# Performance work log

Hardware: AMD Instinct MI355X
Metric: run time of the kernel (lower is better)

## Reference

```python
import jax, jax.numpy as jnp
import numpy as np
import math

HID = 768
HEADS = 12
HEAD_DIM = HID // HEADS
B, L = 64, 1024


def _xavier(key, shape):
    fan_in, fan_out = shape[0], shape[1]
    lim = math.sqrt(6.0 / (fan_in + fan_out))
    return jax.random.uniform(key, shape, jnp.float32, -lim, lim)


def setup_inputs() -> dict:
    key = jax.random.key(0)
    ks = jax.random.split(key, 12)
    inp = {
        "x_img": jax.random.normal(ks[0], (B, L, HID), jnp.float32),
        "cond": jax.random.normal(ks[1], (B, HID), jnp.float32),
        # attention projections
        "wq": _xavier(ks[2], (HID, HID)), "bq": jnp.zeros((HID,), jnp.float32),
        "wk": _xavier(ks[3], (HID, HID)), "bk": jnp.zeros((HID,), jnp.float32),
        "wv": _xavier(ks[4], (HID, HID)), "bv": jnp.zeros((HID,), jnp.float32),
        "wo": _xavier(ks[5], (HID, HID)), "bo": jnp.zeros((HID,), jnp.float32),
        # adaLN: zero-initialized in the original (keep small random so grads are non-trivial? No — stay faithful: zero init is the module's init, but zero would kill modulation. Use small random for a meaningful test.)
        "w_ada": jax.random.normal(ks[6], (HID, 6 * HID), jnp.float32) * 0.02,
        "b_ada": jnp.zeros((6 * HID,), jnp.float32),
        # MLP
        "w1": _xavier(ks[7], (HID, HID)), "b1": jnp.zeros((HID,), jnp.float32),
        "w2": _xavier(ks[8], (HID, HID)), "b2": jnp.zeros((HID,), jnp.float32),
        # LayerNorm params (norm_1: default scale=1, bias init const 1; norm_2: scale init const 1, bias default 0)
        "ln1_scale": jnp.ones((HID,), jnp.float32), "ln1_bias": jnp.ones((HID,), jnp.float32),
        "ln2_scale": jnp.ones((HID,), jnp.float32), "ln2_bias": jnp.zeros((HID,), jnp.float32),
    }
    return inp


def _layernorm(x, scale, bias, eps=1e-6):
    mu = jnp.mean(x, axis=-1, keepdims=True)
    var = jnp.var(x, axis=-1, keepdims=True)
    return (x - mu) * jax.lax.rsqrt(var + eps) * scale + bias


def _modulate(x, shift, scale):
    # shift/scale: [B, H] -> broadcast over seq axis
    return x * (1.0 + scale[:, None, :]) + shift[:, None, :]


def _attention(x, wq, bq, wk, bk, wv, bv, wo, bo):
    q = x @ wq + bq
    k = x @ wk + bk
    v = x @ wv + bv
    def split(t):
        b, l, _ = t.shape
        return t.reshape(b, l, HEADS, HEAD_DIM).transpose(0, 2, 1, 3)  # b h l d
    q, k, v = split(q), split(k), split(v)
    logits = jnp.einsum("bhqd,bhkd->bhqk", q, k) / math.sqrt(HEAD_DIM)
    attn = jax.nn.softmax(logits, axis=-1)
    out = jnp.einsum("bhqk,bhkd->bhqd", attn, v)
    out = out.transpose(0, 2, 1, 3).reshape(x.shape)  # b l (h d)
    return out @ wo + bo


def reference(x_img, cond, wq, bq, wk, bk, wv, bv, wo, bo, w_ada, b_ada,
              w1, b1, w2, b2, ln1_scale, ln1_bias, ln2_scale, ln2_bias):
    c = jax.nn.silu(cond) @ w_ada + b_ada  # [B, 6H]
    shift_msa, scale_msa, gate_msa, shift_mlp, scale_mlp, gate_mlp = jnp.split(c, 6, axis=1)

    h = _modulate(_layernorm(x_img, ln1_scale, ln1_bias), shift_msa, scale_msa)
    attn_out = _attention(h, wq, bq, wk, bk, wv, bv, wo, bo)
    x = x_img + gate_msa[:, None, :] * attn_out

    h2 = _modulate(_layernorm(x, ln2_scale, ln2_bias), shift_mlp, scale_mlp)
    mlp_out = jax.nn.silu(h2 @ w1 + b1) @ w2 + b2
    x = x + gate_mlp[:, None, :] * mlp_out
    return x
```

## Files before the change

### kernel.cpp

```cpp
#include <hip/hip_runtime.h>
#include <hip/hip_bf16.h>

typedef __bf16 bf16x8 __attribute__((ext_vector_type(8)));
typedef __bf16 bf16x4 __attribute__((ext_vector_type(4)));
typedef float  f32x4  __attribute__((ext_vector_type(4)));

#define MFMA_BF16(A_, B_, C_) __builtin_amdgcn_mfma_f32_16x16x32_bf16(A_, B_, C_, 0, 0, 0)

static constexpr int    HIDC  = 768;
static constexpr int    BB    = 64;
static constexpr int    LL    = 1024;
static constexpr int    MROWS = BB * LL;
static constexpr int    NHEAD = 12;
static constexpr int    HD    = 64;
static constexpr size_t QKV1  = (size_t)BB * NHEAD * LL * HD;

static constexpr size_t OFF_WQKVT = 0;
static constexpr size_t OFF_WOT   = OFF_WQKVT + (size_t)2304 * 768 * 2;
static constexpr size_t OFF_W1T   = OFF_WOT   + (size_t)768 * 768 * 2;
static constexpr size_t OFF_W2T   = OFF_W1T   + (size_t)768 * 768 * 2;
static constexpr size_t OFF_BQKV  = OFF_W2T   + (size_t)768 * 768 * 2;
static constexpr size_t OFF_C     = OFF_BQKV  + (size_t)2304 * 4;
static constexpr size_t OFF_H     = OFF_C     + (size_t)64 * 4608 * 4;
static constexpr size_t OFF_AO    = OFF_H     + (size_t)MROWS * HIDC * 2;
static constexpr size_t OFF_QKV   = OFF_AO    + (size_t)MROWS * HIDC * 2;

__device__ __forceinline__ void async16(const __bf16* g, __bf16* l) {
    __builtin_amdgcn_global_load_lds((const __attribute__((address_space(1))) void*)g,
                                     (__attribute__((address_space(3))) void*)l, 16, 0, 0);
}

#define PH_BARRIER() do { __builtin_amdgcn_sched_barrier(0); asm volatile("" ::: "memory"); \
    __builtin_amdgcn_s_barrier(); asm volatile("" ::: "memory"); __builtin_amdgcn_sched_barrier(0); } while (0)

__global__ __launch_bounds__(256) void tcvt_k(const float* __restrict__ src, __bf16* __restrict__ dst) {
    int i = blockIdx.x * 256 + threadIdx.x;
    int kk = i / 768, n = i - kk * 768;
    dst[(size_t)n * 768 + kk] = (__bf16)src[i];
}

__global__ __launch_bounds__(256) void bcat_k(const float* __restrict__ bq, const float* __restrict__ bk,
                                              const float* __restrict__ bv, float* __restrict__ bqkv) {
    int i = blockIdx.x * 256 + threadIdx.x;
    if (i < 2304) {
        int w = i / 768, r = i - w * 768;
        const float* p = (w == 0) ? bq : (w == 1) ? bk : bv;
        bqkv[i] = p[r];
    }
}

__global__ __launch_bounds__(256) void ada_k(const float* __restrict__ cond, const float* __restrict__ w_ada,
                                             const float* __restrict__ b_ada, float* __restrict__ c) {
    __shared__ float s[8][768];
    const int tid = threadIdx.x;
    const int bt = blockIdx.x / 18;
    const int nt = blockIdx.x % 18;
    #pragma unroll
    for (int i = 0; i < 24; ++i) {
        int idx = i * 256 + tid;
        int bb = idx / 768, kk = idx - bb * 768;
        float v = cond[(size_t)(bt * 8 + bb) * 768 + kk];
        s[bb][kk] = v / (1.f + __expf(-v));
    }
    __syncthreads();
    const int n = nt * 256 + tid;
    float acc[8];
    #pragma unroll
    for (int j = 0; j < 8; ++j) acc[j] = 0.f;
    for (int k = 0; k < 768; ++k) {
        float w = w_ada[(size_t)k * 4608 + n];
        #pragma unroll
        for (int j = 0; j < 8; ++j) acc[j] += s[j][k] * w;
    }
    float bias = b_ada[n];
    #pragma unroll
    for (int j = 0; j < 8; ++j) c[(size_t)(bt * 8 + j) * 4608 + n] = acc[j] + bias;
}

__global__ __launch_bounds__(256) void ln_mod_k(const float* __restrict__ x,
                                                const float* __restrict__ lns, const float* __restrict__ lnb,
                                                const float* __restrict__ c, int shift_off, int scale_off,
                                                __bf16* __restrict__ out) {
    const int row = blockIdx.x, tid = threadIdx.x;
    const size_t base = (size_t)row * HIDC;
    const int b = row >> 10;
    float v0 = x[base + tid], v1 = x[base + 256 + tid], v2 = x[base + 512 + tid];
    float s = v0 + v1 + v2;
    float ss = v0 * v0 + v1 * v1 + v2 * v2;
    #pragma unroll
    for (int off = 1; off < 64; off <<= 1) { s += __shfl_xor(s, off); ss += __shfl_xor(ss, off); }
    __shared__ float red[8];
    const int wave = tid >> 6, lane = tid & 63;
    if (lane == 0) { red[wave] = s; red[4 + wave] = ss; }
    __syncthreads();
    s  = red[0] + red[1] + red[2] + red[3];
    ss = red[4] + red[5] + red[6] + red[7];
    const float mu   = s * (1.f / 768.f);
    const float var  = ss * (1.f / 768.f) - mu * mu;
    const float rstd = rsqrtf(var + 1e-6f);
    const float* cb = c + (size_t)b * 4608;
    #pragma unroll
    for (int i = 0; i < 3; ++i) {
        int col = i * 256 + tid;
        float v = (i == 0) ? v0 : (i == 1) ? v1 : v2;
        float val = (v - mu) * rstd * lns[col] + lnb[col];
        val = val * (1.f + cb[scale_off + col]) + cb[shift_off + col];
        out[base + col] = (__bf16)val;
    }
}

__global__ __launch_bounds__(256) void vtr_k(const __bf16* __restrict__ v, __bf16* __restrict__ vt) {
    __shared__ __attribute__((aligned(16))) __bf16 t[64][72];
    const int bid = blockIdx.x;
    const int bh = bid >> 4, lt = bid & 15;
    const int l0 = lt * 64;
    const size_t src = (size_t)bh * LL * HD + (size_t)l0 * HD;
    const size_t dst = (size_t)bh * HD * LL + l0;
    const int tid = threadIdx.x;
    const int rA = tid >> 3, cA = (tid & 7) * 8;
    bf16x8 a0 = *(const bf16x8*)(v + src + (size_t)rA * HD + cA);
    bf16x8 a1 = *(const bf16x8*)(v + src + (size_t)(rA + 32) * HD + cA);
    *(bf16x8*)&t[rA][cA] = a0;
    *(bf16x8*)&t[rA + 32][cA] = a1;
    __syncthreads();
    const int r2 = tid & 31, dg = tid >> 5;
    bf16x8 b0 = *(const bf16x8*)&t[2 * r2][dg * 8];
    bf16x8 b1 = *(const bf16x8*)&t[2 * r2 + 1][dg * 8];
    #pragma unroll
    for (int j = 0; j < 8; ++j) {
        union { __bf16 h[2]; unsigned u; } pk;
        pk.h[0] = b0[j]; pk.h[1] = b1[j];
        *reinterpret_cast<unsigned*>(vt + dst + (size_t)(dg * 8 + j) * LL + 2 * r2) = pk.u;
    }
}

template<int EPI>
__global__ __launch_bounds__(512, 2) void gemm256_k(const __bf16* __restrict__ A, const __bf16* __restrict__ BT,
                                                    const float* __restrict__ bias, int NBLK,
                                                    const float* __restrict__ e_res, const float* __restrict__ e_gate,
                                                    void* __restrict__ out0) {
    constexpr int K = 768;
    constexpr int NKT = K / 64;
    __shared__ __attribute__((aligned(16))) unsigned char LDSB[131072];
    const int tid = threadIdx.x;
    const int nwg = gridDim.x;
    const int cpx = nwg >> 3;
    const int bid = blockIdx.x;
    const int swz = (bid & 7) * cpx + (bid >> 3);
    const int mb = swz / NBLK, nb = swz - mb * NBLK;
    const size_t m0 = (size_t)mb * 256;
    const int n0 = nb * 256;
    const int wave = tid >> 6, lane = tid & 63;
    const int wm = wave >> 2, wn = wave & 3;
    const int lr = lane & 15, lg = lane >> 4;

    int prow[2], pcol[2], pphys[2];
    #pragma unroll
    for (int i = 0; i < 2; ++i) {
        int p = (i * 512 + tid) * 16;
        int Lb = p ^ (((p >> 9) & 1) << 5);
        prow[i] = Lb >> 7;
        pcol[i] = (Lb & 127) >> 1;
        pphys[i] = p;
    }
    auto STAGE = [&](const __bf16* gbase, size_t rowstart, int kt, int regoff) {
        #pragma unroll
        for (int i = 0; i < 2; ++i) {
            const __bf16* g = gbase + (rowstart + (size_t)prow[i]) * K + kt * 64 + pcol[i];
            async16(g, (__bf16*)(LDSB + regoff + pphys[i]));
        }
    };
    auto AFRAG = [&](int db, int mf, int ks) -> bf16x8 {
        int Lb = (mf * 16 + lr) * 128 + ks * 64 + lg * 16;
        int ph = Lb ^ (((Lb >> 9) & 1) << 5);
        return *(const bf16x8*)(LDSB + db * 65536 + wm * 16384 + ph);
    };
    auto BFRAG = [&](int db, int nf, int ks) -> bf16x8 {
        int Lb = ((wn & 1) * 64 + nf * 16 + lr) * 128 + ks * 64 + lg * 16;
        int ph = Lb ^ (((Lb >> 9) & 1) << 5);
        return *(const bf16x8*)(LDSB + db * 65536 + 32768 + (wn >> 1) * 16384 + ph);
    };

    f32x4 acc[8][4];
    #pragma unroll
    for (int i = 0; i < 8; ++i)
        #pragma unroll
        for (int j = 0; j < 4; ++j) acc[i][j] = (f32x4){0.f, 0.f, 0.f, 0.f};
    bf16x8 Af[4][2], Bf[4][2];

    STAGE(BT, (size_t)n0,       0, 32768);
    STAGE(BT, (size_t)n0 + 128, 0, 49152);
    STAGE(A,  m0,               0, 0);
    STAGE(A,  m0 + 128,         0, 16384);
    STAGE(BT, (size_t)n0,       1, 65536 + 32768);
    STAGE(BT, (size_t)n0 + 128, 1, 65536 + 49152);
    asm volatile("s_waitcnt vmcnt(4)" ::: "memory");
    PH_BARRIER();

    #pragma unroll 2
    for (int g = 0; g < NKT; ++g) {
        const int db = g & 1, dbn = db ^ 1;
        if (g + 1 < NKT) STAGE(A, m0, g + 1, dbn * 65536);
        #pragma unroll
        for (int mf = 0; mf < 4; ++mf) { Af[mf][0] = AFRAG(db, mf, 0); Af[mf][1] = AFRAG(db, mf, 1); }
        #pragma unroll
        for (int nf = 0; nf < 2; ++nf) { Bf[nf][0] = BFRAG(db, nf, 0); Bf[nf][1] = BFRAG(db, nf, 1); }
        __builtin_amdgcn_s_setprio(1);
        #pragma unroll
        for (int ks = 0; ks < 2; ++ks)
            #pragma unroll
            for (int mf = 0; mf < 4; ++mf)
                #pragma unroll
                for (int nf = 0; nf < 2; ++nf)
                    acc[mf][nf] = MFMA_BF16(Af[mf][ks], Bf[nf][ks], acc[mf][nf]);
        __builtin_amdgcn_s_setprio(0);
        PH_BARRIER();
        if (g + 1 < NKT) STAGE(A, m0 + 128, g + 1, dbn * 65536 + 16384);
        #pragma unroll
        for (int nf = 2; nf < 4; ++nf) { Bf[nf][0] = BFRAG(db, nf, 0); Bf[nf][1] = BFRAG(db, nf, 1); }
        __builtin_amdgcn_s_setprio(1);
        #pragma unroll
        for (int ks = 0; ks < 2; ++ks)
            #pragma unroll
            for (int mf = 0; mf < 4; ++mf)
                #pragma unroll
                for (int nf = 2; nf < 4; ++nf)
                    acc[mf][nf] = MFMA_BF16(Af[mf][ks], Bf[nf][ks], acc[mf][nf]);
        __builtin_amdgcn_s_setprio(0);
        PH_BARRIER();
        if (g + 2 < NKT) STAGE(BT, (size_t)n0, g + 2, db * 65536 + 32768);
        #pragma unroll
        for (int mf = 0; mf < 4; ++mf) { Af[mf][0] = AFRAG(db, mf + 4, 0); Af[mf][1] = AFRAG(db, mf + 4, 1); }
        __builtin_amdgcn_s_setprio(1);
        #pragma unroll
        for (int ks = 0; ks < 2; ++ks)
            #pragma unroll
            for (int mf = 0; mf < 4; ++mf)
                #pragma unroll
                for (int nf = 0; nf < 2; ++nf)
                    acc[mf + 4][nf] = MFMA_BF16(Af[mf][ks], Bf[nf][ks], acc[mf + 4][nf]);
        __builtin_amdgcn_s_setprio(0);
        PH_BARRIER();
        if (g + 2 < NKT) STAGE(BT, (size_t)n0 + 128, g + 2, db * 65536 + 49152);
        __builtin_amdgcn_s_setprio(1);
        #pragma unroll
        for (int ks = 0; ks < 2; ++ks)
            #pragma unroll
            for (int mf = 0; mf < 4; ++mf)
                #pragma unroll
                for (int nf = 2; nf < 4; ++nf)
                    acc[mf + 4][nf] = MFMA_BF16(Af[mf][ks], Bf[nf][ks], acc[mf + 4][nf]);
        __builtin_amdgcn_s_setprio(0);
        if (g < NKT - 2)       asm volatile("s_waitcnt vmcnt(4)" ::: "memory");
        else if (g == NKT - 2) asm volatile("s_waitcnt vmcnt(0)" ::: "memory");
        if (g + 1 < NKT) PH_BARRIER();
    }

    #pragma unroll
    for (int mf = 0; mf < 8; ++mf) {
        #pragma unroll
        for (int nf = 0; nf < 4; ++nf) {
            #pragma unroll
            for (int r = 0; r < 4; ++r) {
                const int row = wm * 128 + mf * 16 + lg * 4 + r;
                const int col = wn * 64 + nf * 16 + lr;
                const size_t m = m0 + row;
                const int n = n0 + col;
                float val = acc[mf][nf][r] + bias[n];
                if constexpr (EPI == 0) {
                    int which = n / 768, rem = n - which * 768;
                    int hh = rem >> 6, dd = rem & 63;
                    size_t bI = m >> 10, lI = m & 1023;
                    ((__bf16*)out0)[((((size_t)which * BB + bI) * NHEAD + hh) * LL + lI) * HD + dd] = (__bf16)val;
                } else if constexpr (EPI == 1) {
                    size_t bI = m >> 10;
                    float gg = e_gate[bI * 4608 + n];
                    ((float*)out0)[m * HIDC + n] = e_res[m * HIDC + n] + gg * val;
                } else {
                    float sv = val / (1.f + __expf(-val));
                    ((__bf16*)out0)[m * HIDC + n] = (__bf16)sv;
                }
            }
        }
    }
}

__global__ __launch_bounds__(256) void attn_k(const __bf16* __restrict__ qb, const __bf16* __restrict__ kb,
                                              const __bf16* __restrict__ vtg, __bf16* __restrict__ out) {
    __shared__ __attribute__((aligned(16))) __bf16 Kls[64][72];
    __shared__ __attribute__((aligned(16))) __bf16 Vls[64][72];
    const int nwg = gridDim.x;
    const int cpx = nwg >> 3;
    const int bid = blockIdx.x;
    const int swz = (bid & 7) * cpx + (bid >> 3);
    const int bh = swz >> 3;
    const int qt = swz & 7;
    const int b = bh / NHEAD, h = bh - b * NHEAD;
    const int tid = threadIdx.x;
    const int wave = tid >> 6, lane = tid & 63;
    const int lr = lane & 15, lg = lane >> 4;
    const size_t base  = (size_t)bh * LL * HD;
    const size_t baseT = (size_t)bh * HD * LL;

    const int q0 = qt * 128 + wave * 32;
    bf16x8 qf[2][2];
    #pragma unroll
    for (int qi = 0; qi < 2; ++qi) {
        const __bf16* qrow = qb + base + (size_t)(q0 + qi * 16 + lr) * HD;
        qf[qi][0] = *(const bf16x8*)(qrow + lg * 8);
        qf[qi][1] = *(const bf16x8*)(qrow + 32 + lg * 8);
    }

    f32x4 acc[2][4];
    #pragma unroll
    for (int qi = 0; qi < 2; ++qi)
        #pragma unroll
        for (int i = 0; i < 4; ++i) acc[qi][i] = (f32x4){0.f, 0.f, 0.f, 0.f};
    float m_run[2] = {-1e30f, -1e30f}, l_run[2] = {0.f, 0.f};

    const int rA = tid >> 3, cA = (tid & 7) * 8;

    for (int it = 0; it < LL / 64; ++it) {
        const int kv0 = it * 64;
        bf16x8 rk0 = *(const bf16x8*)(kb + base + (size_t)(kv0 + rA) * HD + cA);
        bf16x8 rk1 = *(const bf16x8*)(kb + base + (size_t)(kv0 + rA + 32) * HD + cA);
        bf16x8 rv0 = *(const bf16x8*)(vtg + baseT + (size_t)rA * LL + kv0 + cA);
        bf16x8 rv1 = *(const bf16x8*)(vtg + baseT + (size_t)(rA + 32) * LL + kv0 + cA);
        __syncthreads();
        *(bf16x8*)&Kls[rA][cA] = rk0;
        *(bf16x8*)&Kls[rA + 32][cA] = rk1;
        *(bf16x8*)&Vls[rA][cA] = rv0;
        *(bf16x8*)&Vls[rA + 32][cA] = rv1;
        __syncthreads();

        f32x4 s[2][4];
        #pragma unroll
        for (int sf = 0; sf < 4; ++sf) {
            const bf16x8 kf0 = *(const bf16x8*)&Kls[sf * 16 + lr][lg * 8];
            const bf16x8 kf1 = *(const bf16x8*)&Kls[sf * 16 + lr][32 + lg * 8];
            #pragma unroll
            for (int qi = 0; qi < 2; ++qi) {
                f32x4 t = (f32x4){0.f, 0.f, 0.f, 0.f};
                t = MFMA_BF16(kf0, qf[qi][0], t);
                t = MFMA_BF16(kf1, qf[qi][1], t);
                s[qi][sf] = t;
            }
        }
        float corr[2];
        #pragma unroll
        for (int qi = 0; qi < 2; ++qi) {
            float tm = -1e30f;
            #pragma unroll
            for (int sf = 0; sf < 4; ++sf)
                #pragma unroll
                for (int r = 0; r < 4; ++r) { float v = s[qi][sf][r] * 0.125f; s[qi][sf][r] = v; tm = fmaxf(tm, v); }
            tm = fmaxf(tm, __shfl_xor(tm, 16));
            tm = fmaxf(tm, __shfl_xor(tm, 32));
            const float mnew = fmaxf(m_run[qi], tm);
            corr[qi] = __expf(m_run[qi] - mnew);
            float rs = 0.f;
            #pragma unroll
            for (int sf = 0; sf < 4; ++sf)
                #pragma unroll
                for (int r = 0; r < 4; ++r) { float e = __expf(s[qi][sf][r] - mnew); s[qi][sf][r] = e; rs += e; }
            rs += __shfl_xor(rs, 16);
            rs += __shfl_xor(rs, 32);
            l_run[qi] = l_run[qi] * corr[qi] + rs;
            m_run[qi] = mnew;
            #pragma unroll
            for (int of = 0; of < 4; ++of)
                #pragma unroll
                for (int r = 0; r < 4; ++r) acc[qi][of][r] *= corr[qi];
        }
        #pragma unroll
        for (int ks = 0; ks < 2; ++ks) {
            bf16x8 pb[2];
            #pragma unroll
            for (int qi = 0; qi < 2; ++qi)
                #pragma unroll
                for (int j = 0; j < 4; ++j) {
                    pb[qi][j]     = (__bf16)s[qi][2 * ks][j];
                    pb[qi][4 + j] = (__bf16)s[qi][2 * ks + 1][j];
                }
            #pragma unroll
            for (int of = 0; of < 4; ++of) {
                const bf16x4 v0 = *(const bf16x4*)&Vls[of * 16 + lr][ks * 32 + lg * 4];
                const bf16x4 v1 = *(const bf16x4*)&Vls[of * 16 + lr][ks * 32 + 16 + lg * 4];
                bf16x8 vf;
                #pragma unroll
                for (int j = 0; j < 4; ++j) { vf[j] = v0[j]; vf[4 + j] = v1[j]; }
                #pragma unroll
                for (int qi = 0; qi < 2; ++qi)
                    acc[qi][of] = MFMA_BF16(vf, pb[qi], acc[qi][of]);
            }
        }
    }
    #pragma unroll
    for (int qi = 0; qi < 2; ++qi) {
        const float inv = 1.f / l_run[qi];
        const int qq = q0 + qi * 16 + lr;
        #pragma unroll
        for (int of = 0; of < 4; ++of)
            #pragma unroll
            for (int r = 0; r < 4; ++r) {
                const int d = of * 16 + lg * 4 + r;
                out[((size_t)b * LL + qq) * HIDC + h * HD + d] = (__bf16)(acc[qi][of][r] * inv);
            }
    }
}

extern "C" void kernel_launch(void* const* d_in, const int* in_sizes, int n_in,
                              void* d_out, int out_size, void* d_ws, size_t ws_size,
                              hipStream_t stream) {
    const float* x_img = (const float*)d_in[0];
    const float* cond  = (const float*)d_in[1];
    const float* wq    = (const float*)d_in[2];
    const float* bq    = (const float*)d_in[3];
    const float* wk    = (const float*)d_in[4];
    const float* bk    = (const float*)d_in[5];
    const float* wv    = (const float*)d_in[6];
    const float* bv    = (const float*)d_in[7];
    const float* wo    = (const float*)d_in[8];
    const float* bo    = (const float*)d_in[9];
    const float* w_ada = (const float*)d_in[10];
    const float* b_ada = (const float*)d_in[11];
    const float* w1    = (const float*)d_in[12];
    const float* b1    = (const float*)d_in[13];
    const float* w2    = (const float*)d_in[14];
    const float* b2    = (const float*)d_in[15];
    const float* ln1s  = (const float*)d_in[16];
    const float* ln1b  = (const float*)d_in[17];
    const float* ln2s  = (const float*)d_in[18];
    const float* ln2b  = (const float*)d_in[19];

    char* ws = (char*)d_ws;
    __bf16* wqkvT = (__bf16*)(ws + OFF_WQKVT);
    __bf16* woT   = (__bf16*)(ws + OFF_WOT);
    __bf16* w1T   = (__bf16*)(ws + OFF_W1T);
    __bf16* w2T   = (__bf16*)(ws + OFF_W2T);
    float*  bqkv  = (float*)(ws + OFF_BQKV);
    float*  cbuf  = (float*)(ws + OFF_C);
    __bf16* hbuf  = (__bf16*)(ws + OFF_H);
    __bf16* vtb   = (__bf16*)(ws + OFF_H);
    __bf16* aobuf = (__bf16*)(ws + OFF_AO);
    __bf16* qkv   = (__bf16*)(ws + OFF_QKV);
    float*  xbuf  = (float*)(ws + OFF_QKV);

    dim3 blk(256);
    dim3 blk512(512);

    tcvt_k<<<2304, blk, 0, stream>>>(wq, wqkvT);
    tcvt_k<<<2304, blk, 0, stream>>>(wk, wqkvT + (size_t)768 * 768);
    tcvt_k<<<2304, blk, 0, stream>>>(wv, wqkvT + (size_t)2 * 768 * 768);
    tcvt_k<<<2304, blk, 0, stream>>>(wo, woT);
    tcvt_k<<<2304, blk, 0, stream>>>(w1, w1T);
    tcvt_k<<<2304, blk, 0, stream>>>(w2, w2T);
    bcat_k<<<9, blk, 0, stream>>>(bq, bk, bv, bqkv);
    ada_k<<<144, blk, 0, stream>>>(cond, w_ada, b_ada, cbuf);

    ln_mod_k<<<MROWS, blk, 0, stream>>>(x_img, ln1s, ln1b, cbuf, 0, 768, hbuf);

    gemm256_k<0><<<2304, blk512, 0, stream>>>(hbuf, wqkvT, bqkv, 9, nullptr, nullptr, (void*)qkv);

    vtr_k<<<768 * 16, blk, 0, stream>>>(qkv + 2 * QKV1, vtb);

    attn_k<<<BB * NHEAD * 8, blk, 0, stream>>>(qkv, qkv + QKV1, vtb, aobuf);

    gemm256_k<1><<<768, blk512, 0, stream>>>(aobuf, woT, bo, 3, x_img, cbuf + 2 * 768, (void*)xbuf);

    ln_mod_k<<<MROWS, blk, 0, stream>>>(xbuf, ln2s, ln2b, cbuf, 3 * 768, 4 * 768, hbuf);

    gemm256_k<2><<<768, blk512, 0, stream>>>(hbuf, w1T, b1, 3, nullptr, nullptr, (void*)aobuf);

    gemm256_k<1><<<768, blk512, 0, stream>>>(aobuf, w2T, b2, 3, xbuf, cbuf + 5 * 768, d_out);

    (void)in_sizes; (void)n_in; (void)out_size; (void)ws_size;
}
```

Baseline: 1.349 ms.

## Pipeline attention K/V loads asynchronously, fuse V layout into QKV epilogue, lazy rescale

The QKV GEMM epilogue now pre-scales Q by log2(e)/sqrt(d), so the softmax can use exp2 directly. It also writes V in an MFMA-fragment-friendly tiled layout, which removes the separate V transpose kernel. The attention kernel stages K and V tiles into a 4-deep LDS ring with async global-to-LDS loads, two tiles ahead, and uses an XOR swizzle on K. It skips the running-max rescale when the new max does not exceed the old one by more than a threshold. The six weight-conversion launches are merged into one. The lazy rescale relies on the threshold keeping exp2 values bounded in fp32.

```diff
diff --git a/kernel.cpp b/kernel.cpp
--- a/kernel.cpp
+++ b/kernel.cpp
@@ -2,7 +2,6 @@
 #include <hip/hip_bf16.h>
 
 typedef __bf16 bf16x8 __attribute__((ext_vector_type(8)));
-typedef __bf16 bf16x4 __attribute__((ext_vector_type(4)));
 typedef float  f32x4  __attribute__((ext_vector_type(4)));
 
 #define MFMA_BF16(A_, B_, C_) __builtin_amdgcn_mfma_f32_16x16x32_bf16(A_, B_, C_, 0, 0, 0)
@@ -14,6 +13,8 @@
 static constexpr int    NHEAD = 12;
 static constexpr int    HD    = 64;
 static constexpr size_t QKV1  = (size_t)BB * NHEAD * LL * HD;
+static constexpr float  QSCALE = 0.1803368801111204f;
+static constexpr float  THR2   = 11.5416f;
 
 static constexpr size_t OFF_WQKVT = 0;
 static constexpr size_t OFF_WOT   = OFF_WQKVT + (size_t)2304 * 768 * 2;
@@ -33,10 +34,16 @@
 #define PH_BARRIER() do { __builtin_amdgcn_sched_barrier(0); asm volatile("" ::: "memory"); \
     __builtin_amdgcn_s_barrier(); asm volatile("" ::: "memory"); __builtin_amdgcn_sched_barrier(0); } while (0)
 
-__global__ __launch_bounds__(256) void tcvt_k(const float* __restrict__ src, __bf16* __restrict__ dst) {
-    int i = blockIdx.x * 256 + threadIdx.x;
+__global__ __launch_bounds__(256) void tcvt6_k(const float* __restrict__ s0, const float* __restrict__ s1,
+                                               const float* __restrict__ s2, const float* __restrict__ s3,
+                                               const float* __restrict__ s4, const float* __restrict__ s5,
+                                               __bf16* __restrict__ dbase) {
+    const int widx = blockIdx.x / 2304;
+    const int i = (blockIdx.x % 2304) * 256 + threadIdx.x;
+    const float* src = (widx == 0) ? s0 : (widx == 1) ? s1 : (widx == 2) ? s2
+                     : (widx == 3) ? s3 : (widx == 4) ? s4 : s5;
     int kk = i / 768, n = i - kk * 768;
-    dst[(size_t)n * 768 + kk] = (__bf16)src[i];
+    dbase[(size_t)widx * 768 * 768 + (size_t)n * 768 + kk] = (__bf16)src[i];
 }
 
 __global__ __launch_bounds__(256) void bcat_k(const float* __restrict__ bq, const float* __restrict__ bk,
@@ -106,31 +113,6 @@
         float val = (v - mu) * rstd * lns[col] + lnb[col];
         val = val * (1.f + cb[scale_off + col]) + cb[shift_off + col];
         out[base + col] = (__bf16)val;
-    }
-}
-
-__global__ __launch_bounds__(256) void vtr_k(const __bf16* __restrict__ v, __bf16* __restrict__ vt) {
-    __shared__ __attribute__((aligned(16))) __bf16 t[64][72];
-    const int bid = blockIdx.x;
-    const int bh = bid >> 4, lt = bid & 15;
-    const int l0 = lt * 64;
-    const size_t src = (size_t)bh * LL * HD + (size_t)l0 * HD;
-    const size_t dst = (size_t)bh * HD * LL + l0;
-    const int tid = threadIdx.x;
-    const int rA = tid >> 3, cA = (tid & 7) * 8;
-    bf16x8 a0 = *(const bf16x8*)(v + src + (size_t)rA * HD + cA);
-    bf16x8 a1 = *(const bf16x8*)(v + src + (size_t)(rA + 32) * HD + cA);
-    *(bf16x8*)&t[rA][cA] = a0;
-    *(bf16x8*)&t[rA + 32][cA] = a1;
-    __syncthreads();
-    const int r2 = tid & 31, dg = tid >> 5;
-    bf16x8 b0 = *(const bf16x8*)&t[2 * r2][dg * 8];
-    bf16x8 b1 = *(const bf16x8*)&t[2 * r2 + 1][dg * 8];
-    #pragma unroll
-    for (int j = 0; j < 8; ++j) {
-        union { __bf16 h[2]; unsigned u; } pk;
-        pk.h[0] = b0[j]; pk.h[1] = b1[j];
-        *reinterpret_cast<unsigned*>(vt + dst + (size_t)(dg * 8 + j) * LL + 2 * r2) = pk.u;
     }
 }
 
@@ -271,7 +253,18 @@
                     int which = n / 768, rem = n - which * 768;
                     int hh = rem >> 6, dd = rem & 63;
                     size_t bI = m >> 10, lI = m & 1023;
-                    ((__bf16*)out0)[((((size_t)which * BB + bI) * NHEAD + hh) * LL + lI) * HD + dd] = (__bf16)val;
+                    if (which == 0) {
+                        ((__bf16*)out0)[(((size_t)bI * NHEAD + hh) * LL + lI) * HD + dd] = (__bf16)(val * QSCALE);
+                    } else if (which == 1) {
+                        ((__bf16*)out0)[QKV1 + (((size_t)bI * NHEAD + hh) * LL + lI) * HD + dd] = (__bf16)val;
+                    } else {
+                        int tile = (int)(lI >> 6), r6 = (int)(lI & 63);
+                        int ks = r6 >> 5, rem2 = r6 & 31;
+                        int lgj = (rem2 & 15) >> 2;
+                        int j = (rem2 & 3) + ((rem2 >> 4) << 2);
+                        ((__bf16*)out0)[2 * QKV1 + ((size_t)bI * NHEAD + hh) * (LL * HD) + (size_t)tile * 4096
+                                        + ((ks * 64 + dd) * 4 + lgj) * 8 + j] = (__bf16)val;
+                    }
                 } else if constexpr (EPI == 1) {
                     size_t bI = m >> 10;
                     float gg = e_gate[bI * 4608 + n];
@@ -286,9 +279,8 @@
 }
 
 __global__ __launch_bounds__(256) void attn_k(const __bf16* __restrict__ qb, const __bf16* __restrict__ kb,
-                                              const __bf16* __restrict__ vtg, __bf16* __restrict__ out) {
-    __shared__ __attribute__((aligned(16))) __bf16 Kls[64][72];
-    __shared__ __attribute__((aligned(16))) __bf16 Vls[64][72];
+                                              const __bf16* __restrict__ v2g, __bf16* __restrict__ out) {
+    __shared__ __attribute__((aligned(16))) unsigned char LDSA[65536];
     const int nwg = gridDim.x;
     const int cpx = nwg >> 3;
     const int bid = blockIdx.x;
@@ -299,8 +291,7 @@
     const int tid = threadIdx.x;
     const int wave = tid >> 6, lane = tid & 63;
     const int lr = lane & 15, lg = lane >> 4;
-    const size_t base  = (size_t)bh * LL * HD;
-    const size_t baseT = (size_t)bh * HD * LL;
+    const size_t base = (size_t)bh * LL * HD;
 
     const int q0 = qt * 128 + wave * 32;
     bf16x8 qf[2][2];
@@ -310,6 +301,30 @@
         qf[qi][0] = *(const bf16x8*)(qrow + lg * 8);
         qf[qi][1] = *(const bf16x8*)(qrow + 32 + lg * 8);
     }
+    __builtin_amdgcn_sched_barrier(0);
+
+    int krow[2], kcol[2];
+    #pragma unroll
+    for (int i = 0; i < 2; ++i) {
+        int p = (i * 256 + tid) * 16;
+        krow[i] = p >> 7;
+        kcol[i] = (p & 127) ^ ((krow[i] & 7) << 4);
+    }
+    auto STAGE = [&](int t) {
+        unsigned char* Lb = LDSA + (t & 3) * 16384;
+        const int kv0 = t * 64;
+        #pragma unroll
+        for (int i = 0; i < 2; ++i) {
+            const __bf16* g = kb + base + (size_t)(kv0 + krow[i]) * HD + (kcol[i] >> 1);
+            async16(g, (__bf16*)(Lb + (i * 256 + tid) * 16));
+        }
+        #pragma unroll
+        for (int i = 0; i < 2; ++i) {
+            int p = (i * 256 + tid) * 16;
+            const __bf16* g = v2g + base + (size_t)t * 4096 + (p >> 1);
+            async16(g, (__bf16*)(Lb + 8192 + p));
+        }
+    };
 
     f32x4 acc[2][4];
     #pragma unroll
@@ -318,59 +333,72 @@
         for (int i = 0; i < 4; ++i) acc[qi][i] = (f32x4){0.f, 0.f, 0.f, 0.f};
     float m_run[2] = {-1e30f, -1e30f}, l_run[2] = {0.f, 0.f};
 
-    const int rA = tid >> 3, cA = (tid & 7) * 8;
-
-    for (int it = 0; it < LL / 64; ++it) {
-        const int kv0 = it * 64;
-        bf16x8 rk0 = *(const bf16x8*)(kb + base + (size_t)(kv0 + rA) * HD + cA);
-        bf16x8 rk1 = *(const bf16x8*)(kb + base + (size_t)(kv0 + rA + 32) * HD + cA);
-        bf16x8 rv0 = *(const bf16x8*)(vtg + baseT + (size_t)rA * LL + kv0 + cA);
-        bf16x8 rv1 = *(const bf16x8*)(vtg + baseT + (size_t)(rA + 32) * LL + kv0 + cA);
-        __syncthreads();
-        *(bf16x8*)&Kls[rA][cA] = rk0;
-        *(bf16x8*)&Kls[rA + 32][cA] = rk1;
-        *(bf16x8*)&Vls[rA][cA] = rv0;
-        *(bf16x8*)&Vls[rA + 32][cA] = rv1;
-        __syncthreads();
+    STAGE(0);
+    STAGE(1);
+
+    for (int t = 0; t < LL / 64; ++t) {
+        if (t + 2 < LL / 64) {
+            STAGE(t + 2);
+            asm volatile("s_waitcnt vmcnt(8)" ::: "memory");
+        } else if (t + 2 == LL / 64) {
+            asm volatile("s_waitcnt vmcnt(4)" ::: "memory");
+        } else {
+            asm volatile("s_waitcnt vmcnt(0)" ::: "memory");
+        }
+        PH_BARRIER();
+        const unsigned char* KB = LDSA + (t & 3) * 16384;
+        const unsigned char* VB = KB + 8192;
 
         f32x4 s[2][4];
         #pragma unroll
         for (int sf = 0; sf < 4; ++sf) {
-            const bf16x8 kf0 = *(const bf16x8*)&Kls[sf * 16 + lr][lg * 8];
-            const bf16x8 kf1 = *(const bf16x8*)&Kls[sf * 16 + lr][32 + lg * 8];
+            const int row = sf * 16 + lr;
+            const bf16x8 kf0 = *(const bf16x8*)(KB + row * 128 + ((lg * 16) ^ ((row & 7) << 4)));
+            const bf16x8 kf1 = *(const bf16x8*)(KB + row * 128 + ((64 + lg * 16) ^ ((row & 7) << 4)));
             #pragma unroll
             for (int qi = 0; qi < 2; ++qi) {
-                f32x4 t = (f32x4){0.f, 0.f, 0.f, 0.f};
-                t = MFMA_BF16(kf0, qf[qi][0], t);
-                t = MFMA_BF16(kf1, qf[qi][1], t);
-                s[qi][sf] = t;
+                f32x4 tt = (f32x4){0.f, 0.f, 0.f, 0.f};
+                tt = MFMA_BF16(kf0, qf[qi][0], tt);
+                tt = MFMA_BF16(kf1, qf[qi][1], tt);
+                s[qi][sf] = tt;
             }
         }
-        float corr[2];
+        float tm[2];
         #pragma unroll
         for (int qi = 0; qi < 2; ++qi) {
-            float tm = -1e30f;
+            float v = -1e30f;
             #pragma unroll
             for (int sf = 0; sf < 4; ++sf)
                 #pragma unroll
-                for (int r = 0; r < 4; ++r) { float v = s[qi][sf][r] * 0.125f; s[qi][sf][r] = v; tm = fmaxf(tm, v); }
-            tm = fmaxf(tm, __shfl_xor(tm, 16));
-            tm = fmaxf(tm, __shfl_xor(tm, 32));
-            const float mnew = fmaxf(m_run[qi], tm);
-            corr[qi] = __expf(m_run[qi] - mnew);
+                for (int r = 0; r < 4; ++r) v = fmaxf(v, s[qi][sf][r]);
+            v = fmaxf(v, __shfl_xor(v, 16));
+            v = fmaxf(v, __shfl_xor(v, 32));
+            tm[qi] = v;
+        }
+        const int skip = __all((tm[0] - m_run[0] <= THR2) && (tm[1] - m_run[1] <= THR2));
+        if (!skip) {
+            #pragma unroll
+            for (int qi = 0; qi < 2; ++qi) {
+                const float mnew = fmaxf(m_run[qi], tm[qi]);
+                const float corr = exp2f(m_run[qi] - mnew);
+                l_run[qi] *= corr;
+                #pragma unroll
+                for (int of = 0; of < 4; ++of)
+                    #pragma unroll
+                    for (int r = 0; r < 4; ++r) acc[qi][of][r] *= corr;
+                m_run[qi] = mnew;
+            }
+        }
+        #pragma unroll
+        for (int qi = 0; qi < 2; ++qi) {
             float rs = 0.f;
             #pragma unroll
             for (int sf = 0; sf < 4; ++sf)
                 #pragma unroll
-                for (int r = 0; r < 4; ++r) { float e = __expf(s[qi][sf][r] - mnew); s[qi][sf][r] = e; rs += e; }
+                for (int r = 0; r < 4; ++r) { float e = exp2f(s[qi][sf][r] - m_run[qi]); s[qi][sf][r] = e; rs += e; }
             rs += __shfl_xor(rs, 16);
             rs += __shfl_xor(rs, 32);
-            l_run[qi] = l_run[qi] * corr[qi] + rs;
-            m_run[qi] = mnew;
-            #pragma unroll
-            for (int of = 0; of < 4; ++of)
-                #pragma unroll
-                for (int r = 0; r < 4; ++r) acc[qi][of][r] *= corr[qi];
+            l_run[qi] += rs;
         }
         #pragma unroll
         for (int ks = 0; ks < 2; ++ks) {
@@ -384,11 +412,7 @@
                 }
             #pragma unroll
             for (int of = 0; of < 4; ++of) {
-                const bf16x4 v0 = *(const bf16x4*)&Vls[of * 16 + lr][ks * 32 + lg * 4];
-                const bf16x4 v1 = *(const bf16x4*)&Vls[of * 16 + lr][ks * 32 + 16 + lg * 4];
-                bf16x8 vf;
-                #pragma unroll
-                for (int j = 0; j < 4; ++j) { vf[j] = v0[j]; vf[4 + j] = v1[j]; }
+                const bf16x8 vf = *(const bf16x8*)(VB + ((ks * 64 + of * 16 + lr) * 4 + lg) * 16);
                 #pragma unroll
                 for (int qi = 0; qi < 2; ++qi)
                     acc[qi][of] = MFMA_BF16(vf, pb[qi], acc[qi][of]);
@@ -441,7 +465,6 @@
     float*  bqkv  = (float*)(ws + OFF_BQKV);
     float*  cbuf  = (float*)(ws + OFF_C);
     __bf16* hbuf  = (__bf16*)(ws + OFF_H);
-    __bf16* vtb   = (__bf16*)(ws + OFF_H);
     __bf16* aobuf = (__bf16*)(ws + OFF_AO);
     __bf16* qkv   = (__bf16*)(ws + OFF_QKV);
     float*  xbuf  = (float*)(ws + OFF_QKV);
@@ -449,12 +472,7 @@
     dim3 blk(256);
     dim3 blk512(512);
 
-    tcvt_k<<<2304, blk, 0, stream>>>(wq, wqkvT);
-    tcvt_k<<<2304, blk, 0, stream>>>(wk, wqkvT + (size_t)768 * 768);
-    tcvt_k<<<2304, blk, 0, stream>>>(wv, wqkvT + (size_t)2 * 768 * 768);
-    tcvt_k<<<2304, blk, 0, stream>>>(wo, woT);
-    tcvt_k<<<2304, blk, 0, stream>>>(w1, w1T);
-    tcvt_k<<<2304, blk, 0, stream>>>(w2, w2T);
+    tcvt6_k<<<6 * 2304, blk, 0, stream>>>(wq, wk, wv, wo, w1, w2, wqkvT);
     bcat_k<<<9, blk, 0, stream>>>(bq, bk, bv, bqkv);
     ada_k<<<144, blk, 0, stream>>>(cond, w_ada, b_ada, cbuf);
 
@@ -462,9 +480,7 @@
 
     gemm256_k<0><<<2304, blk512, 0, stream>>>(hbuf, wqkvT, bqkv, 9, nullptr, nullptr, (void*)qkv);
 
-    vtr_k<<<768 * 16, blk, 0, stream>>>(qkv + 2 * QKV1, vtb);
-
-    attn_k<<<BB * NHEAD * 8, blk, 0, stream>>>(qkv, qkv + QKV1, vtb, aobuf);
+    attn_k<<<BB * NHEAD * 8, blk, 0, stream>>>(qkv, qkv + QKV1, qkv + 2 * QKV1, aobuf);
 
     gemm256_k<1><<<768, blk512, 0, stream>>>(aobuf, woT, bo, 3, x_img, cbuf + 2 * 768, (void*)xbuf);
 
```

Measured after the change: 1.445 ms. +7.2%, slower.
